# Kernel optimization log

Hardware: AMD Instinct MI355X
Metric: run time of the kernel (lower is better)

Reference implementation:

```python
import jax, jax.numpy as jnp
import numpy as np

B, T, C, H = 4, 2048, 2048, 16
HD = C // H  # head_dim = 128


def setup_inputs() -> dict:
    key = jax.random.key(0)
    k1, k2, k3 = jax.random.split(key, 3)
    x = jax.random.normal(k1, (B, T, C), dtype=jnp.float32)
    w_qkv = jax.random.normal(k2, (C, 3 * C), dtype=jnp.float32) * (C ** -0.5)
    w_proj = jax.random.normal(k3, (C, C), dtype=jnp.float32) * (C ** -0.5)
    return {"x": x, "w_qkv": w_qkv, "w_proj": w_proj}


def reference(x, w_qkv, w_proj):
    Bx, Tx, Cx = x.shape
    qkv = x @ w_qkv                       # [B, T, 3C]
    q, k, v = jnp.split(qkv, 3, axis=-1)  # each [B, T, C]

    def split_heads(t):
        return t.reshape(Bx, Tx, H, HD).transpose(0, 2, 1, 3)  # [B, H, T, HD]

    q, k, v = split_heads(q), split_heads(k), split_heads(v)
    scale = HD ** -0.5
    attn = jnp.einsum("bhqd,bhkd->bhqk", q, k) * scale  # [B, H, T, T]
    causal = jnp.tril(jnp.ones((Tx, Tx), dtype=bool))
    attn = jnp.where(causal[None, None], attn, -jnp.inf)
    attn = jax.nn.softmax(attn, axis=-1)
    out = jnp.einsum("bhqk,bhkd->bhqd", attn, v)        # [B, H, T, HD]
    out = out.transpose(0, 2, 1, 3).reshape(Bx, Tx, Cx)  # [B, T, C]
    return out @ w_proj
```

## Files before the change

### kernel.cpp

```cpp
#include <hip/hip_runtime.h>
#include <hip/hip_bf16.h>
#include <math.h>

typedef __bf16 bf16;
typedef __bf16 bf16x8 __attribute__((ext_vector_type(8)));
typedef float f32x4 __attribute__((ext_vector_type(4)));

#define AS1(p) ((const __attribute__((address_space(1))) void*)(p))
#define AS3(p) ((__attribute__((address_space(3))) void*)(p))

__device__ __forceinline__ void gl_lds16(const bf16* g, bf16* l) {
    __builtin_amdgcn_global_load_lds(AS1(g), AS3(l), 16, 0, 0);
}

__global__ __launch_bounds__(256) void cast_f32_bf16(const float* __restrict__ in,
                                                     bf16* __restrict__ out, long n) {
    long i = ((long)blockIdx.x * 256 + threadIdx.x) * 4;
    if (i + 3 < n) {
        float4 v = *(const float4*)(in + i);
        out[i + 0] = (bf16)v.x;
        out[i + 1] = (bf16)v.y;
        out[i + 2] = (bf16)v.z;
        out[i + 3] = (bf16)v.w;
    }
}

__global__ __launch_bounds__(256) void transpose_cast(const float* __restrict__ in,
                                                      bf16* __restrict__ out,
                                                      int R, int Cc) {
    __shared__ float tile[32][33];
    const int t = threadIdx.x;
    const int r0 = blockIdx.y * 32, c0 = blockIdx.x * 32;
    for (int i = 0; i < 4; ++i) {
        int idx = t + i * 256;
        int r = idx >> 5, c = idx & 31;
        tile[r][c] = in[(size_t)(r0 + r) * Cc + c0 + c];
    }
    __syncthreads();
    for (int i = 0; i < 4; ++i) {
        int idx = t + i * 256;
        int r = idx >> 5, c = idx & 31;
        out[(size_t)(c0 + r) * R + r0 + c] = (bf16)tile[c][r];
    }
}

template <typename OT>
__global__ __launch_bounds__(512, 2) void gemm256_bt(const bf16* __restrict__ A,
                                                     const bf16* __restrict__ BT,
                                                     OT* __restrict__ C,
                                                     int M, int N, int K) {
    __shared__ bf16 lds[2][2][256 * 64];
    const int t = threadIdx.x;
    const int lane = t & 63;
    const int w = t >> 6;
    const int wr = w >> 2, wc = w & 3;
    const int l15 = lane & 15, lg = lane >> 4;

    const int nbx = gridDim.x, nby = gridDim.y;
    const int orig = blockIdx.y * nbx + blockIdx.x;
    const int span = nby * 8;
    const int grp = orig / span, rem = orig % span;
    const int bm = rem >> 3, bn = grp * 8 + (rem & 7);

    const bf16* Ab = A + (size_t)bm * 256 * K;
    const bf16* Bb = BT + (size_t)bn * 256 * K;

    f32x4 acc[8][4] = {};

    const int nk = K / 64;
    int cur = 0;
    for (int j = 0; j < 4; ++j) {
        int cid = j * 512 + t;
        int r = cid >> 3, c = cid & 7;
        int src = (c ^ (r & 7)) << 3;
        gl_lds16(Ab + (size_t)r * K + src, &lds[0][0][cid * 8]);
        gl_lds16(Bb + (size_t)r * K + src, &lds[0][1][cid * 8]);
    }

    for (int kt = 0; kt < nk; ++kt) {
        __syncthreads();

        if (kt + 1 < nk) {
            const int k0 = (kt + 1) * 64;
            for (int j = 0; j < 4; ++j) {
                int cid = j * 512 + t;
                int r = cid >> 3, c = cid & 7;
                int src = (c ^ (r & 7)) << 3;
                gl_lds16(Ab + (size_t)r * K + k0 + src, &lds[cur ^ 1][0][cid * 8]);
                gl_lds16(Bb + (size_t)r * K + k0 + src, &lds[cur ^ 1][1][cid * 8]);
            }
        }

        const bf16* lA = &lds[cur][0][0];
        const bf16* lB = &lds[cur][1][0];
        bf16x8 bfrag[2][4];
        for (int kk = 0; kk < 2; ++kk)
            for (int n = 0; n < 4; ++n) {
                int R = wc * 64 + n * 16 + l15;
                bfrag[kk][n] = *(const bf16x8*)(lB + R * 64 + (((kk * 4 + lg) ^ (R & 7)) << 3));
            }
        int R0 = wr * 128 + l15;
        bf16x8 a0 = *(const bf16x8*)(lA + R0 * 64 + ((lg ^ (R0 & 7)) << 3));
        bf16x8 a1 = *(const bf16x8*)(lA + R0 * 64 + (((4 + lg) ^ (R0 & 7)) << 3));
        __builtin_amdgcn_s_setprio(1);
        for (int m = 0; m < 8; ++m) {
            bf16x8 c0 = a0, c1 = a1;
            if (m + 1 < 8) {
                int Rn = wr * 128 + (m + 1) * 16 + l15;
                a0 = *(const bf16x8*)(lA + Rn * 64 + ((lg ^ (Rn & 7)) << 3));
                a1 = *(const bf16x8*)(lA + Rn * 64 + (((4 + lg) ^ (Rn & 7)) << 3));
            }
            for (int n = 0; n < 4; ++n) {
                acc[m][n] = __builtin_amdgcn_mfma_f32_16x16x32_bf16(c0, bfrag[0][n], acc[m][n], 0, 0, 0);
                acc[m][n] = __builtin_amdgcn_mfma_f32_16x16x32_bf16(c1, bfrag[1][n], acc[m][n], 0, 0, 0);
            }
        }
        __builtin_amdgcn_s_setprio(0);
        cur ^= 1;
    }

    for (int m = 0; m < 8; ++m)
        for (int n = 0; n < 4; ++n) {
            int row = bm * 256 + wr * 128 + m * 16 + lg * 4;
            int col = bn * 256 + wc * 64 + n * 16 + l15;
            for (int r = 0; r < 4; ++r)
                C[(size_t)(row + r) * N + col] = (OT)acc[m][n][r];
        }
}

__global__ __launch_bounds__(256, 2) void attn_fwd(const bf16* __restrict__ QKV,
                                                   bf16* __restrict__ O) {
    __shared__ bf16 lK[64 * 128];
    __shared__ bf16 lVt[128 * 64];
    __shared__ bf16 lP[4][32 * 68];

    const int t = threadIdx.x, lane = t & 63, w = t >> 6;
    const int l15 = lane & 15, lg = lane >> 4;
    const int bh = blockIdx.y;
    const int b = bh >> 4, h = bh & 15;
    const size_t rs = 6144;

    const bf16* Qb = QKV + (size_t)b * 2048 * rs + h * 128;
    const bf16* Kb = Qb + 2048;
    const bf16* Vb = Qb + 4096;

    const float C = 0.12751705f;
    const int kvp = t & 31;
    const int hd0 = (t >> 5) * 16;

    for (int half = 0; half < 2; ++half) {
        const int qt = half == 0 ? (15 - (int)blockIdx.x) : (int)blockIdx.x;
        const int q0 = qt * 128;
        const int qa = q0 + w * 32;

        bf16x8 qf[2][4];
        for (int f = 0; f < 2; ++f)
            for (int kk = 0; kk < 4; ++kk) {
                bf16x8 q = *(const bf16x8*)(Qb + (size_t)(qa + f * 16 + l15) * rs + kk * 32 + lg * 8);
                for (int e = 0; e < 8; ++e) q[e] = (bf16)((float)q[e] * C);
                qf[f][kk] = q;
            }

        f32x4 o[2][8] = {};
        float m2[2][4], l2[2][4];
        for (int f = 0; f < 2; ++f)
            for (int r = 0; r < 4; ++r) { m2[f][r] = -1e30f; l2[f][r] = 0.f; }

        const int nt = q0 / 64 + 2;

        for (int j = 0; j < 4; ++j) {
            int c = j * 256 + t;
            int r = c >> 4, cc = c & 15;
            gl_lds16(Kb + (size_t)r * rs + ((cc ^ (r & 7)) << 3), lK + (size_t)c * 8);
        }
        bf16x8 vr0, vr1, vr2, vr3;
        {
            const bf16* p = Vb + (size_t)(2 * kvp) * rs + hd0;
            vr0 = *(const bf16x8*)(p);
            vr1 = *(const bf16x8*)(p + rs);
            vr2 = *(const bf16x8*)(p + 8);
            vr3 = *(const bf16x8*)(p + rs + 8);
        }

        for (int kt = 0; kt < nt; ++kt) {
            const int kv0 = kt * 64;
            __syncthreads();

            for (int e = 0; e < 8; ++e) {
                union { bf16 h2[2]; unsigned u; } p0, p1;
                p0.h2[0] = vr0[e]; p0.h2[1] = vr1[e];
                p1.h2[0] = vr2[e]; p1.h2[1] = vr3[e];
                int r0 = hd0 + e, r1 = hd0 + 8 + e;
                *(unsigned*)(lVt + r0 * 64 + (((kvp >> 2) ^ (r0 & 7)) << 3) + ((kvp & 3) << 1)) = p0.u;
                *(unsigned*)(lVt + r1 * 64 + (((kvp >> 2) ^ (r1 & 7)) << 3) + ((kvp & 3) << 1)) = p1.u;
            }

            f32x4 s[2][4] = {};
            __builtin_amdgcn_s_setprio(1);
            for (int n = 0; n < 4; ++n) {
                int row = n * 16 + l15;
                for (int kk = 0; kk < 4; ++kk) {
                    bf16x8 kf = *(const bf16x8*)(lK + row * 128 + (((kk * 4 + lg) ^ (row & 7)) << 3));
                    s[0][n] = __builtin_amdgcn_mfma_f32_16x16x32_bf16(qf[0][kk], kf, s[0][n], 0, 0, 0);
                    s[1][n] = __builtin_amdgcn_mfma_f32_16x16x32_bf16(qf[1][kk], kf, s[1][n], 0, 0, 0);
                }
            }
            __builtin_amdgcn_s_setprio(0);

            float pv[2][4][4];
            if (kv0 + 63 <= qa) {
                for (int f = 0; f < 2; ++f)
                    for (int n = 0; n < 4; ++n)
                        for (int r = 0; r < 4; ++r)
                            pv[f][n][r] = s[f][n][r];
            } else {
                for (int f = 0; f < 2; ++f)
                    for (int n = 0; n < 4; ++n)
                        for (int r = 0; r < 4; ++r) {
                            int qg = qa + f * 16 + lg * 4 + r;
                            int kg = kv0 + n * 16 + l15;
                            pv[f][n][r] = (kg <= qg) ? s[f][n][r] : -1e30f;
                        }
            }
            float pmax[2][4];
            for (int f = 0; f < 2; ++f)
                for (int r = 0; r < 4; ++r)
                    pmax[f][r] = fmaxf(fmaxf(pv[f][0][r], pv[f][1][r]), fmaxf(pv[f][2][r], pv[f][3][r]));
            for (int d = 1; d < 16; d <<= 1)
                for (int f = 0; f < 2; ++f)
                    for (int r = 0; r < 4; ++r)
                        pmax[f][r] = fmaxf(pmax[f][r], __shfl_xor(pmax[f][r], d));
            bool need = false;
            for (int f = 0; f < 2; ++f)
                for (int r = 0; r < 4; ++r)
                    need = need || (pmax[f][r] > m2[f][r] + 8.f);
            if (__any(need ? 1 : 0)) {
                for (int f = 0; f < 2; ++f)
                    for (int r = 0; r < 4; ++r) {
                        float mn = fmaxf(m2[f][r], pmax[f][r]);
                        float al = exp2f(m2[f][r] - mn);
                        m2[f][r] = mn;
                        l2[f][r] *= al;
                        for (int j = 0; j < 8; ++j) o[f][j][r] *= al;
                    }
            }
            for (int f = 0; f < 2; ++f)
                for (int n = 0; n < 4; ++n)
                    for (int r = 0; r < 4; ++r) {
                        float p = exp2f(pv[f][n][r] - m2[f][r]);
                        l2[f][r] += p;
                        lP[w][(f * 16 + lg * 4 + r) * 68 + n * 16 + l15] = (bf16)p;
                    }
            bf16x8 pf[2][2];
            for (int f = 0; f < 2; ++f) {
                pf[f][0] = *(const bf16x8*)(&lP[w][(f * 16 + l15) * 68 + lg * 8]);
                pf[f][1] = *(const bf16x8*)(&lP[w][(f * 16 + l15) * 68 + 32 + lg * 8]);
            }

            __syncthreads();

            if (kt + 1 < nt) {
                const int nk2 = kv0 + 64;
                for (int j = 0; j < 4; ++j) {
                    int c = j * 256 + t;
                    int r = c >> 4, cc = c & 15;
                    gl_lds16(Kb + (size_t)(nk2 + r) * rs + ((cc ^ (r & 7)) << 3), lK + (size_t)c * 8);
                }
                const bf16* p = Vb + (size_t)(nk2 + 2 * kvp) * rs + hd0;
                vr0 = *(const bf16x8*)(p);
                vr1 = *(const bf16x8*)(p + rs);
                vr2 = *(const bf16x8*)(p + 8);
                vr3 = *(const bf16x8*)(p + rs + 8);
            }

            __builtin_amdgcn_s_setprio(1);
            for (int j = 0; j < 8; ++j) {
                int R = j * 16 + l15;
                bf16x8 vfa = *(const bf16x8*)(lVt + R * 64 + ((lg ^ (R & 7)) << 3));
                bf16x8 vfb = *(const bf16x8*)(lVt + R * 64 + (((4 + lg) ^ (R & 7)) << 3));
                o[0][j] = __builtin_amdgcn_mfma_f32_16x16x32_bf16(pf[0][0], vfa, o[0][j], 0, 0, 0);
                o[0][j] = __builtin_amdgcn_mfma_f32_16x16x32_bf16(pf[0][1], vfb, o[0][j], 0, 0, 0);
                o[1][j] = __builtin_amdgcn_mfma_f32_16x16x32_bf16(pf[1][0], vfa, o[1][j], 0, 0, 0);
                o[1][j] = __builtin_amdgcn_mfma_f32_16x16x32_bf16(pf[1][1], vfb, o[1][j], 0, 0, 0);
            }
            __builtin_amdgcn_s_setprio(0);
        }

        for (int d = 1; d < 16; d <<= 1)
            for (int f = 0; f < 2; ++f)
                for (int r = 0; r < 4; ++r)
                    l2[f][r] += __shfl_xor(l2[f][r], d);
        for (int f = 0; f < 2; ++f) {
            float inv[4];
            for (int r = 0; r < 4; ++r) inv[r] = 1.f / l2[f][r];
            bf16* Ob = O + ((size_t)b * 2048 + qa + f * 16) * 2048 + h * 128;
            for (int j = 0; j < 8; ++j)
                for (int r = 0; r < 4; ++r)
                    Ob[(size_t)(lg * 4 + r) * 2048 + j * 16 + l15] = (bf16)(o[f][j][r] * inv[r]);
        }
    }
}

extern "C" void kernel_launch(void* const* d_in, const int* in_sizes, int n_in,
                              void* d_out, int out_size, void* d_ws, size_t ws_size,
                              hipStream_t stream) {
    const float* x     = (const float*)d_in[0];
    const float* wqkv  = (const float*)d_in[1];
    const float* wproj = (const float*)d_in[2];
    float* out = (float*)d_out;

    char* ws = (char*)d_ws;
    bf16* xb     = (bf16*)(ws);
    bf16* wqkvT  = (bf16*)(ws + 33554432);
    bf16* wprojT = (bf16*)(ws + 33554432 + 25165824);
    bf16* QKV    = (bf16*)(ws + 33554432 + 25165824 + 8388608);
    bf16* Obuf   = xb;

    cast_f32_bf16<<<dim3(16384), 256, 0, stream>>>(x, xb, (long)8192 * 2048);
    transpose_cast<<<dim3(192, 64), 256, 0, stream>>>(wqkv, wqkvT, 2048, 6144);
    transpose_cast<<<dim3(64, 64), 256, 0, stream>>>(wproj, wprojT, 2048, 2048);
    gemm256_bt<bf16><<<dim3(24, 32), 512, 0, stream>>>(xb, wqkvT, QKV, 8192, 6144, 2048);
    attn_fwd<<<dim3(8, 64), 256, 0, stream>>>(QKV, Obuf);
    gemm256_bt<float><<<dim3(8, 32), 512, 0, stream>>>(Obuf, wprojT, out, 8192, 2048, 2048);
}
```

Baseline: 457.1 us.

## Switch GEMM inner loop to 32x32x16 MFMA with staggered row order

The 256x256 GEMM tile now uses 32x32x16 bf16 MFMA instructions instead of 16x16x32, so each wave holds four by two 32x32 accumulators and the fragment loads and epilogue index mapping are redone to match. Waves in the upper half of the block walk the M sub-tiles in a rotated order, which spreads out LDS bank and instruction contention. The larger MFMA shape needs fewer LDS fragment reads per FLOP. The A fragments are no longer prefetched one step ahead, which may expose LDS latency.

```diff
diff --git a/kernel.cpp b/kernel.cpp
--- a/kernel.cpp
+++ b/kernel.cpp
@@ -5,6 +5,7 @@
 typedef __bf16 bf16;
 typedef __bf16 bf16x8 __attribute__((ext_vector_type(8)));
 typedef float f32x4 __attribute__((ext_vector_type(4)));
+typedef float f32x16 __attribute__((ext_vector_type(16)));
 
 #define AS1(p) ((const __attribute__((address_space(1))) void*)(p))
 #define AS3(p) ((__attribute__((address_space(3))) void*)(p))
@@ -54,7 +55,7 @@
     const int lane = t & 63;
     const int w = t >> 6;
     const int wr = w >> 2, wc = w & 3;
-    const int l15 = lane & 15, lg = lane >> 4;
+    const int l31 = lane & 31, lh = lane >> 5;
 
     const int nbx = gridDim.x, nby = gridDim.y;
     const int orig = blockIdx.y * nbx + blockIdx.x;
@@ -65,7 +66,7 @@
     const bf16* Ab = A + (size_t)bm * 256 * K;
     const bf16* Bb = BT + (size_t)bn * 256 * K;
 
-    f32x4 acc[8][4] = {};
+    f32x16 acc[4][2] = {};
 
     const int nk = K / 64;
     int cur = 0;
@@ -94,37 +95,55 @@
         const bf16* lA = &lds[cur][0][0];
         const bf16* lB = &lds[cur][1][0];
         bf16x8 bfrag[2][4];
-        for (int kk = 0; kk < 2; ++kk)
-            for (int n = 0; n < 4; ++n) {
-                int R = wc * 64 + n * 16 + l15;
-                bfrag[kk][n] = *(const bf16x8*)(lB + R * 64 + (((kk * 4 + lg) ^ (R & 7)) << 3));
-            }
-        int R0 = wr * 128 + l15;
-        bf16x8 a0 = *(const bf16x8*)(lA + R0 * 64 + ((lg ^ (R0 & 7)) << 3));
-        bf16x8 a1 = *(const bf16x8*)(lA + R0 * 64 + (((4 + lg) ^ (R0 & 7)) << 3));
+        #pragma unroll
+        for (int nb = 0; nb < 2; ++nb)
+            #pragma unroll
+            for (int ks = 0; ks < 4; ++ks) {
+                int R = wc * 64 + nb * 32 + l31;
+                int ch = ks * 2 + lh;
+                bfrag[nb][ks] = *(const bf16x8*)(lB + R * 64 + ((ch ^ (R & 7)) << 3));
+            }
         __builtin_amdgcn_s_setprio(1);
-        for (int m = 0; m < 8; ++m) {
-            bf16x8 c0 = a0, c1 = a1;
-            if (m + 1 < 8) {
-                int Rn = wr * 128 + (m + 1) * 16 + l15;
-                a0 = *(const bf16x8*)(lA + Rn * 64 + ((lg ^ (Rn & 7)) << 3));
-                a1 = *(const bf16x8*)(lA + Rn * 64 + (((4 + lg) ^ (Rn & 7)) << 3));
-            }
-            for (int n = 0; n < 4; ++n) {
-                acc[m][n] = __builtin_amdgcn_mfma_f32_16x16x32_bf16(c0, bfrag[0][n], acc[m][n], 0, 0, 0);
-                acc[m][n] = __builtin_amdgcn_mfma_f32_16x16x32_bf16(c1, bfrag[1][n], acc[m][n], 0, 0, 0);
+        if (w & 4) {
+            #pragma unroll
+            for (int i = 0; i < 4; ++i) {
+                const int mb = (i + 2) & 3;
+                int R = wr * 128 + mb * 32 + l31;
+                #pragma unroll
+                for (int ks = 0; ks < 4; ++ks) {
+                    int ch = ks * 2 + lh;
+                    bf16x8 af = *(const bf16x8*)(lA + R * 64 + ((ch ^ (R & 7)) << 3));
+                    acc[mb][0] = __builtin_amdgcn_mfma_f32_32x32x16_bf16(af, bfrag[0][ks], acc[mb][0], 0, 0, 0);
+                    acc[mb][1] = __builtin_amdgcn_mfma_f32_32x32x16_bf16(af, bfrag[1][ks], acc[mb][1], 0, 0, 0);
+                }
+            }
+        } else {
+            #pragma unroll
+            for (int i = 0; i < 4; ++i) {
+                const int mb = i;
+                int R = wr * 128 + mb * 32 + l31;
+                #pragma unroll
+                for (int ks = 0; ks < 4; ++ks) {
+                    int ch = ks * 2 + lh;
+                    bf16x8 af = *(const bf16x8*)(lA + R * 64 + ((ch ^ (R & 7)) << 3));
+                    acc[mb][0] = __builtin_amdgcn_mfma_f32_32x32x16_bf16(af, bfrag[0][ks], acc[mb][0], 0, 0, 0);
+                    acc[mb][1] = __builtin_amdgcn_mfma_f32_32x32x16_bf16(af, bfrag[1][ks], acc[mb][1], 0, 0, 0);
+                }
             }
         }
         __builtin_amdgcn_s_setprio(0);
         cur ^= 1;
     }
 
-    for (int m = 0; m < 8; ++m)
-        for (int n = 0; n < 4; ++n) {
-            int row = bm * 256 + wr * 128 + m * 16 + lg * 4;
-            int col = bn * 256 + wc * 64 + n * 16 + l15;
-            for (int r = 0; r < 4; ++r)
-                C[(size_t)(row + r) * N + col] = (OT)acc[m][n][r];
+    for (int mb = 0; mb < 4; ++mb)
+        for (int nb = 0; nb < 2; ++nb) {
+            int colg = bn * 256 + wc * 64 + nb * 32 + l31;
+            #pragma unroll
+            for (int reg = 0; reg < 16; ++reg) {
+                int row = (reg & 3) + 8 * (reg >> 2) + 4 * lh;
+                int rowg = bm * 256 + wr * 128 + mb * 32 + row;
+                C[(size_t)rowg * N + colg] = (OT)acc[mb][nb][reg];
+            }
         }
 }
 
```

Measured after the change: 474.2 us. +3.8%, slower.
